# Optimization experiments

Measured on AMD Instinct MI355X. Metric: run time of the kernel, lower is better.

## Reference

```python
import jax, jax.numpy as jnp
import numpy as np

N, K, D = 65536, 1024, 256


def setup_inputs() -> dict:
    key = jax.random.key(0)
    k1, k2 = jax.random.split(key)
    e = jax.random.normal(k1, (N, D), dtype=jnp.float32)
    # module inits codebook uniform in [-1/K, 1/K]
    weight = jax.random.uniform(k2, (K, D), dtype=jnp.float32,
                                minval=-1.0 / K, maxval=1.0 / K)
    return {"e": e, "weight": weight}


def reference(e, weight):
    distances = (jnp.sum(e * e, axis=1, keepdims=True)
                 - 2.0 * jnp.matmul(e, weight.T)
                 + jnp.sum(weight * weight, axis=1))
    encoding_indices = jnp.argmin(distances, axis=1)            # [N]
    # one-hot @ weight is just a gather
    quantized = weight[encoding_indices]                        # [N, D]
    commitment_loss = jnp.mean((jax.lax.stop_gradient(quantized) - e) ** 2)
    counts = jnp.zeros((K,), dtype=jnp.float32).at[encoding_indices].add(1.0)
    codebook_usage = counts.max() / counts.sum()
    # straight-through estimator
    quantized = e + jax.lax.stop_gradient(quantized - e)
    return quantized, encoding_indices, commitment_loss, codebook_usage
```

## Files before the change

kernel.cpp:

```cpp
#include <hip/hip_runtime.h>

typedef __attribute__((ext_vector_type(8))) short short8;
typedef __attribute__((ext_vector_type(4))) float floatx4;

#define N_ROWS 65536
#define K_CB   1024
#define D_DIM  256

#define TAU 4.0e-4f
#define BLINE 520

#define OFF_WN     262144
#define OFF_FIXCNT 266240
#define OFF_HIST   266496
#define OFF_IDX    270592
#define OFF_LIST   532736
#define OFF_PART   794880
#define OFF_WFRAG  827392
#define OFF_KEYS   1351680
#define OFF_WT     1875968

__device__ __forceinline__ float pw128_sq(const float4* p) {
#pragma clang fp contract(off)
    float4 q0 = p[0], q1 = p[1];
    float r0 = q0.x * q0.x, r1 = q0.y * q0.y, r2 = q0.z * q0.z, r3 = q0.w * q0.w;
    float r4 = q1.x * q1.x, r5 = q1.y * q1.y, r6 = q1.z * q1.z, r7 = q1.w * q1.w;
    for (int i = 1; i < 16; ++i) {
        float4 u0 = p[2 * i], u1 = p[2 * i + 1];
        r0 = r0 + u0.x * u0.x; r1 = r1 + u0.y * u0.y;
        r2 = r2 + u0.z * u0.z; r3 = r3 + u0.w * u0.w;
        r4 = r4 + u1.x * u1.x; r5 = r5 + u1.y * u1.y;
        r6 = r6 + u1.z * u1.z; r7 = r7 + u1.w * u1.w;
    }
    return ((r0 + r1) + (r2 + r3)) + ((r4 + r5) + (r6 + r7));
}
__device__ __forceinline__ float rownorm_np(const float* row) {
#pragma clang fp contract(off)
    float s0 = pw128_sq((const float4*)row);
    float s1 = pw128_sq((const float4*)(row + 128));
    return s0 + s1;
}
__device__ __forceinline__ float np_dist(float A, float m, float Ck) {
#pragma clang fp contract(off)
    float Bv = 2.0f * m;
    float t  = A - Bv;
    return t + Ck;
}
__device__ __forceinline__ unsigned short bf16_rne(float x) {
    unsigned u = __float_as_uint(x);
    unsigned r = u + 0x7fff + ((u >> 16) & 1);
    return (unsigned short)(r >> 16);
}
__device__ __forceinline__ unsigned long long dist_key(float d, int idx) {
    unsigned u = __float_as_uint(d);
    unsigned k32 = u ^ (((unsigned)((int)u >> 31)) | 0x80000000u);
    return ((unsigned long long)k32 << 32) | (unsigned)idx;
}

#define PRS 260
__global__ __launch_bounds__(256) void k_prep(
        const float* __restrict__ wg,
        float* __restrict__ wn,
        unsigned short* __restrict__ wfrag, float* __restrict__ wt) {
    __shared__ __align__(16) float es[32 * PRS];
    const int tid = threadIdx.x;
    const int bx  = blockIdx.x;
    if (bx < 4) {
        int row = bx * 256 + tid;
        wn[row] = rownorm_np(wg + (size_t)row * D_DIM);
    } else if (bx < 132) {
        int t = (bx - 4) * 256 + tid;
        int col = t >> 5, kc = t & 31;
        const float4* src = (const float4*)(wg + (size_t)col * D_DIM + kc * 8);
        float4 v0 = src[0], v1 = src[1];
        const float a[8] = {v0.x, v0.y, v0.z, v0.w, v1.x, v1.y, v1.z, v1.w};
        short8 h;
        #pragma unroll
        for (int i = 0; i < 8; ++i) h[i] = (short)bf16_rne(a[i]);
        *(short8*)(wfrag + ((size_t)kc * 1024 + col) * 8) = h;
    } else {
        float (*tw)[PRS] = (float(*)[PRS])es;
        const int cb = bx - 132;
        const int c0 = cb * 32;
        #pragma unroll
        for (int it = 0; it < 8; ++it) {
            int idx = it * 256 + tid;
            int code = idx >> 6, f4 = idx & 63;
            *(float4*)&tw[code][f4 * 4] =
                *(const float4*)(wg + (size_t)(c0 + code) * D_DIM + f4 * 4);
        }
        __syncthreads();
        const int j = tid & 31, dg = tid >> 5;
        #pragma unroll
        for (int dd = 0; dd < 32; ++dd) {
            int d = dd * 8 + dg;
            wt[(size_t)d * K_CB + c0 + j] = tw[j][d];
        }
    }
}

__global__ __launch_bounds__(256, 2) void k_dist(
        const float* __restrict__ eg, const unsigned short* __restrict__ wfrag,
        const float* __restrict__ wn,
        int* __restrict__ idx_ws, int* __restrict__ fixlist, int* __restrict__ fixcnt) {
    __shared__ __align__(16) unsigned short Bs[2][32 * BLINE];
    __shared__ float wnS[K_CB];
    const int tid  = threadIdx.x;
    const int lane = tid & 63;
    const int wv   = tid >> 6;
    const int q    = lane >> 4;
    const int m15  = lane & 15;
    const int waveRow = blockIdx.x * 128 + wv * 32;

    #pragma unroll
    for (int i = 0; i < 4; ++i) wnS[tid + i * 256] = wn[tid + i * 256];

    short8 afh0[8], afh1[8];
    #pragma unroll
    for (int mt = 0; mt < 2; ++mt) {
        const float* rowp = eg + (size_t)(waveRow + mt * 16 + m15) * D_DIM + q * 8;
        #pragma unroll
        for (int win = 0; win < 8; ++win) {
            const float4* pa = (const float4*)(rowp + win * 32);
            float4 x0 = pa[0], x1 = pa[1];
            const float a[8] = {x0.x, x0.y, x0.z, x0.w, x1.x, x1.y, x1.z, x1.w};
            short8 h;
            #pragma unroll
            for (int i = 0; i < 8; ++i) h[i] = (short)bf16_rne(a[i]);
            if (mt == 0) afh0[win] = h; else afh1[win] = h;
        }
    }

    float best[8], sec[8];
    int bidx[8];
    #pragma unroll
    for (int s = 0; s < 8; ++s) { best[s] = 3.4e38f; sec[s] = 3.4e38f; bidx[s] = 0; }

    #pragma unroll
    for (int t = 0; t < 8; ++t) {
        int L = wv * 8 + t;
        const unsigned short* src = wfrag + ((size_t)L * 1024) * 8 + lane * 8;
        __builtin_amdgcn_global_load_lds(
            (const __attribute__((address_space(1))) unsigned int*)src,
            (__attribute__((address_space(3))) unsigned int*)&Bs[0][L * BLINE],
            16, 0, 0);
    }
    __syncthreads();

    for (int cb = 0; cb < 16; ++cb) {
        const int p = cb & 1;
        if (cb < 15) {
            #pragma unroll
            for (int t = 0; t < 8; ++t) {
                int L = wv * 8 + t;
                const unsigned short* src =
                    wfrag + ((size_t)L * 1024 + (cb + 1) * 64) * 8 + lane * 8;
                __builtin_amdgcn_global_load_lds(
                    (const __attribute__((address_space(1))) unsigned int*)src,
                    (__attribute__((address_space(3))) unsigned int*)&Bs[p ^ 1][L * BLINE],
                    16, 0, 0);
            }
        }
        #pragma unroll
        for (int nt = 0; nt < 4; ++nt) {
            floatx4 acc0 = (floatx4){0.f, 0.f, 0.f, 0.f};
            floatx4 acc1 = (floatx4){0.f, 0.f, 0.f, 0.f};
            #pragma unroll
            for (int win = 0; win < 8; ++win) {
                int kc = win * 4 + q;
                short8 bfh = *(short8*)&Bs[p][kc * BLINE + (nt * 16 + m15) * 8];
                acc0 = __builtin_amdgcn_mfma_f32_16x16x32_bf16(afh0[win], bfh, acc0, 0, 0, 0);
                acc1 = __builtin_amdgcn_mfma_f32_16x16x32_bf16(afh1[win], bfh, acc1, 0, 0, 0);
            }
            int col = cb * 64 + nt * 16 + m15;
            float Ck = wnS[col];
            #pragma unroll
            for (int reg = 0; reg < 4; ++reg) {
                float d0 = __builtin_fmaf(-2.0f, acc0[reg], Ck);
                bool lt0 = d0 < best[reg];
                sec[reg]  = __builtin_amdgcn_fmed3f(d0, best[reg], sec[reg]);
                best[reg] = fminf(d0, best[reg]);
                bidx[reg] = lt0 ? col : bidx[reg];
                float d1 = __builtin_fmaf(-2.0f, acc1[reg], Ck);
                int s1 = 4 + reg;
                bool lt1 = d1 < best[s1];
                sec[s1]  = __builtin_amdgcn_fmed3f(d1, best[s1], sec[s1]);
                best[s1] = fminf(d1, best[s1]);
                bidx[s1] = lt1 ? col : bidx[s1];
            }
        }
        __syncthreads();
    }

    #pragma unroll
    for (int s = 0; s < 8; ++s) {
        float b = best[s], se = sec[s];
        int ix = bidx[s];
        #pragma unroll
        for (int m = 1; m < 16; m <<= 1) {
            float bo = __shfl_xor(b, m, 64);
            float so = __shfl_xor(se, m, 64);
            int   io = __shfl_xor(ix, m, 64);
            float ns = fminf(fminf(se, so), fmaxf(b, bo));
            if (bo < b || (bo == b && io < ix)) { b = bo; ix = io; }
            se = ns;
        }
        if (m15 == 0) {
            int row = waveRow + (s >> 2) * 16 + q * 4 + (s & 3);
            idx_ws[row] = ix;
            if (se - b < TAU) {
                int p = atomicAdd(fixcnt, 1);
                fixlist[p] = row;
            }
        }
    }
}

#define FG_ROWS 8
__global__ __launch_bounds__(256) void k_fixup(
        const float* __restrict__ eg, const float* __restrict__ wg,
        const float* __restrict__ wt, const float* __restrict__ wnorm,
        const int* __restrict__ fixlist, const int* __restrict__ fixcnt,
        unsigned long long* __restrict__ keys) {
    __shared__ __align__(16) float xs[FG_ROWS][D_DIM];
    __shared__ float AnS[FG_ROWS];
    const int tid  = threadIdx.x;
    const int lane = tid & 63;
    const int cnt = *fixcnt;
    if (cnt == 0) return;
    const int ngroups = (cnt + FG_ROWS - 1) / FG_ROWS;
    const int ntiles  = ngroups * 2;
    const int rowg = tid >> 7;
    const int cg   = tid & 127;
    for (int t = blockIdx.x; t < ntiles; t += gridDim.x) {
        const int g     = t >> 1;
        const int chunk = t & 1;
        __syncthreads();
        int rows[FG_ROWS];
        #pragma unroll
        for (int i = 0; i < FG_ROWS; ++i) {
            int j = g * FG_ROWS + i;
            rows[i] = fixlist[j < cnt ? j : cnt - 1];
        }
        #pragma unroll
        for (int i = 0; i < FG_ROWS; ++i)
            xs[i][tid] = eg[(size_t)rows[i] * D_DIM + tid];
        __syncthreads();

        if (tid < 16) {
            int row = tid >> 1, half = tid & 1;
            float sN = pw128_sq((const float4*)&xs[row][half * 128]);
            float so = __shfl_xor(sN, 1, 64);
            if (half == 0) AnS[row] = sN + so;
        }

        const int c0 = chunk * 512 + cg * 4;
        float Cw[4];
        #pragma unroll
        for (int c = 0; c < 4; ++c) Cw[c] = wnorm[c0 + c];

        float s[4][4];
        #pragma unroll
        for (int r = 0; r < 4; ++r)
            #pragma unroll
            for (int c = 0; c < 4; ++c) s[r][c] = 0.f;

        #pragma unroll 2
        for (int d = 0; d < D_DIM; d += 2) {
            float4 wa = *(const float4*)(wt + (size_t)d * K_CB + c0);
            float4 wb = *(const float4*)(wt + (size_t)(d + 1) * K_CB + c0);
            #pragma unroll
            for (int r = 0; r < 4; ++r) {
                float2 e2 = *(const float2*)&xs[rowg * 4 + r][d];
                s[r][0] += e2.x * wa.x + e2.y * wb.x;
                s[r][1] += e2.x * wa.y + e2.y * wb.y;
                s[r][2] += e2.x * wa.z + e2.y * wb.z;
                s[r][3] += e2.x * wa.w + e2.y * wb.w;
            }
        }
        __syncthreads();

        #pragma unroll
        for (int r = 0; r < 4; ++r) {
            const int R = rowg * 4 + r;
            float An = AnS[R];
            unsigned long long kb = 0xFFFFFFFFFFFFFFFFull, ks = 0xFFFFFFFFFFFFFFFFull;
            #pragma unroll
            for (int c = 0; c < 4; ++c) {
                float dq = np_dist(An, s[r][c], Cw[c]);
                unsigned long long kk = dist_key(dq, c0 + c);
                if (kk < kb) { ks = kb; kb = kk; }
                else if (kk < ks) { ks = kk; }
            }
            #pragma unroll
            for (int m = 1; m < 64; m <<= 1) {
                unsigned long long ko = __shfl_xor(kb, m, 64);
                unsigned long long so = __shfl_xor(ks, m, 64);
                if (ko < kb) { ks = (so < kb) ? so : kb; kb = ko; }
                else         { ks = (ko < ks) ? ko : ks; }
            }
            int cand = (int)((lane < 32 ? kb : ks) & 0xFFFFFFFFull);
            const float* wrow = wg + (size_t)cand * D_DIM + (lane & 31) * 8;
            const float* erow = &xs[R][(lane & 31) * 8];
            double sm = 0.0;
            #pragma unroll
            for (int jj = 0; jj < 8; ++jj)
                sm += (double)erow[jj] * (double)wrow[jj];
            #pragma unroll
            for (int m = 1; m < 32; m <<= 1) sm += __shfl_xor(sm, m, 64);
            double smo = __shfl_xor(sm, 32, 64);
            if (lane == 0) {
                int i0 = (int)(kb & 0xFFFFFFFFull);
                int i1 = (int)(ks & 0xFFFFFFFFull);
                float d0 = np_dist(An, (float)sm,  wnorm[i0]);
                float d1 = np_dist(An, (float)smo, wnorm[i1]);
                unsigned long long k0 = dist_key(d0, i0);
                unsigned long long k1 = dist_key(d1, i1);
                unsigned long long kf = k0 < k1 ? k0 : k1;
                int j = g * FG_ROWS + R;
                if (j < cnt) atomicMin(&keys[j], kf);
            }
        }
    }
}

__global__ void k_fixscatter(const int* __restrict__ fixlist, const int* __restrict__ fixcnt,
                             const unsigned long long* __restrict__ keys,
                             int* __restrict__ idx_ws) {
    const int cnt = *fixcnt;
    for (int j = blockIdx.x * blockDim.x + threadIdx.x; j < cnt;
         j += gridDim.x * blockDim.x)
        idx_ws[fixlist[j]] = (int)(keys[j] & 0xFFFFFFFFull);
}

__global__ void k_final(const float* __restrict__ eg, const float* __restrict__ wg,
                        const int* __restrict__ idx_ws, float* __restrict__ qout,
                        float* __restrict__ iout, int* __restrict__ hist,
                        double* __restrict__ partials) {
    const int tid  = threadIdx.x;
    const int sub  = tid >> 6;
    const int lane = tid & 63;
    const int rowBase = blockIdx.x * 16;
    double acc = 0.0;
    #pragma unroll
    for (int g = 0; g < 4; ++g) {
        int row = rowBase + g * 4 + sub;
        int k = idx_ws[row];
        float4 ev = ((const float4*)(eg + (size_t)row * D_DIM))[lane];
        float4 wv = ((const float4*)(wg + (size_t)k   * D_DIM))[lane];
        float dx = wv.x - ev.x, dy = wv.y - ev.y, dz = wv.z - ev.z, dw = wv.w - ev.w;
        float4 qv = {ev.x + dx, ev.y + dy, ev.z + dz, ev.w + dw};
        ((float4*)(qout + (size_t)row * D_DIM))[lane] = qv;
        acc += (double)(dx * dx) + (double)(dy * dy)
             + (double)(dz * dz) + (double)(dw * dw);
        if (lane == 0) {
            iout[row] = (float)k;
            atomicAdd(&hist[k], 1);
        }
    }
    __shared__ double red[256];
    red[tid] = acc;
    __syncthreads();
    for (int st = 128; st > 0; st >>= 1) {
        if (tid < st) red[tid] += red[tid + st];
        __syncthreads();
    }
    if (tid == 0) partials[blockIdx.x] = red[0];
}

__global__ void k_scalars(const int* __restrict__ hist, const double* __restrict__ partials,
                          float* __restrict__ sout) {
    const int tid = threadIdx.x;
    double s = 0.0;
    for (int j = tid; j < N_ROWS / 16; j += 256) s += partials[j];
    int m = 0;
    for (int j = tid; j < K_CB; j += 256) m = max(m, hist[j]);
    __shared__ double rs[256];
    __shared__ int    rm[256];
    rs[tid] = s; rm[tid] = m;
    __syncthreads();
    for (int st = 128; st > 0; st >>= 1) {
        if (tid < st) { rs[tid] += rs[tid + st]; rm[tid] = max(rm[tid], rm[tid + st]); }
        __syncthreads();
    }
    if (tid == 0) {
        sout[0] = (float)(rs[0] / (double)((size_t)N_ROWS * D_DIM));
        sout[1] = (float)rm[0] / 65536.0f;
    }
}

extern "C" void kernel_launch(void* const* d_in, const int* in_sizes, int n_in,
                              void* d_out, int out_size, void* d_ws, size_t ws_size,
                              hipStream_t stream) {
    const float* e = (const float*)d_in[0];
    const float* w = (const float*)d_in[1];
    float* out  = (float*)d_out;
    float* qout = out;
    float* iout = out + (size_t)N_ROWS * D_DIM;
    float* sout = iout + N_ROWS;

    char* ws = (char*)d_ws;
    float*  wn       = (float*) (ws + OFF_WN);
    int*    fixcnt   = (int*)   (ws + OFF_FIXCNT);
    int*    hist     = (int*)   (ws + OFF_HIST);
    int*    idxp     = (int*)   (ws + OFF_IDX);
    int*    list     = (int*)   (ws + OFF_LIST);
    double* partials = (double*)(ws + OFF_PART);
    unsigned short* wfrag = (unsigned short*)(ws + OFF_WFRAG);
    unsigned long long* keys = (unsigned long long*)(ws + OFF_KEYS);
    float*  wt       = (float*) (ws + OFF_WT);

    hipMemsetAsync(ws + OFF_FIXCNT, 0, 4352, stream);
    hipMemsetAsync(ws + OFF_KEYS, 0xFF, 524288, stream);

    hipLaunchKernelGGL(k_prep,       dim3(164),         dim3(256), 0, stream, w, wn, wfrag, wt);
    hipLaunchKernelGGL(k_dist,       dim3(512),         dim3(256), 0, stream, e, wfrag, wn, idxp, list, fixcnt);
    hipLaunchKernelGGL(k_fixup,      dim3(2048),        dim3(256), 0, stream, e, w, wt, wn, list, fixcnt, keys);
    hipLaunchKernelGGL(k_fixscatter, dim3(64),          dim3(256), 0, stream, list, fixcnt, keys, idxp);
    hipLaunchKernelGGL(k_final,      dim3(N_ROWS / 16), dim3(256), 0, stream, e, w, idxp, qout, iout, hist, partials);
    hipLaunchKernelGGL(k_scalars,    dim3(1),           dim3(256), 0, stream, hist, partials, sout);
}
```

Measured before the change: 296.9 us.

## Stage e rows through LDS and interleave MFMA accumulators across column tiles

The A-fragment load now stages each wave's 16 rows into LDS with coalesced global_load_lds, replacing the strided per-lane global reads, then reads the fragments back from LDS. The MFMA loop is restructured so each B fragment feeds 8 independent accumulators (2 row tiles x 4 column tiles). This hides MFMA dependency latency and spreads the LDS reads. The cost is more accumulator registers, which may hurt occupancy under launch_bounds(256,2), plus extra barriers in the prologue.

```diff
diff --git a/kernel.cpp b/kernel.cpp
--- a/kernel.cpp
+++ b/kernel.cpp
@@ -9,6 +9,7 @@
 
 #define TAU 4.0e-4f
 #define BLINE 520
+#define PRS 260
 
 #define OFF_WN     262144
 #define OFF_FIXCNT 266240
@@ -57,7 +58,6 @@
     return ((unsigned long long)k32 << 32) | (unsigned)idx;
 }
 
-#define PRS 260
 __global__ __launch_bounds__(256) void k_prep(
         const float* __restrict__ wg,
         float* __restrict__ wn,
@@ -115,20 +115,32 @@
     #pragma unroll
     for (int i = 0; i < 4; ++i) wnS[tid + i * 256] = wn[tid + i * 256];
 
+    float* ef = (float*)&Bs[0][0];
     short8 afh0[8], afh1[8];
     #pragma unroll
     for (int mt = 0; mt < 2; ++mt) {
-        const float* rowp = eg + (size_t)(waveRow + mt * 16 + m15) * D_DIM + q * 8;
+        #pragma unroll
+        for (int t = 0; t < 16; ++t) {
+            int slot = wv * 16 + t;
+            const float* src = eg + (size_t)(waveRow + mt * 16 + t) * D_DIM + lane * 4;
+            __builtin_amdgcn_global_load_lds(
+                (const __attribute__((address_space(1))) unsigned int*)src,
+                (__attribute__((address_space(3))) unsigned int*)&ef[slot * PRS],
+                16, 0, 0);
+        }
+        __syncthreads();
+        const float* rowp = &ef[(wv * 16 + m15) * PRS + q * 8];
         #pragma unroll
         for (int win = 0; win < 8; ++win) {
-            const float4* pa = (const float4*)(rowp + win * 32);
-            float4 x0 = pa[0], x1 = pa[1];
+            float4 x0 = *(const float4*)(rowp + win * 32);
+            float4 x1 = *(const float4*)(rowp + win * 32 + 4);
             const float a[8] = {x0.x, x0.y, x0.z, x0.w, x1.x, x1.y, x1.z, x1.w};
             short8 h;
             #pragma unroll
             for (int i = 0; i < 8; ++i) h[i] = (short)bf16_rne(a[i]);
             if (mt == 0) afh0[win] = h; else afh1[win] = h;
         }
+        __syncthreads();
     }
 
     float best[8], sec[8];
@@ -161,27 +173,34 @@
                     16, 0, 0);
             }
         }
+        floatx4 acc[2][4];
+        #pragma unroll
+        for (int mt = 0; mt < 2; ++mt)
+            #pragma unroll
+            for (int nt = 0; nt < 4; ++nt)
+                acc[mt][nt] = (floatx4){0.f, 0.f, 0.f, 0.f};
+        #pragma unroll
+        for (int win = 0; win < 8; ++win) {
+            int kc = win * 4 + q;
+            #pragma unroll
+            for (int nt = 0; nt < 4; ++nt) {
+                short8 bfh = *(short8*)&Bs[p][kc * BLINE + (nt * 16 + m15) * 8];
+                acc[0][nt] = __builtin_amdgcn_mfma_f32_16x16x32_bf16(afh0[win], bfh, acc[0][nt], 0, 0, 0);
+                acc[1][nt] = __builtin_amdgcn_mfma_f32_16x16x32_bf16(afh1[win], bfh, acc[1][nt], 0, 0, 0);
+            }
+        }
         #pragma unroll
         for (int nt = 0; nt < 4; ++nt) {
-            floatx4 acc0 = (floatx4){0.f, 0.f, 0.f, 0.f};
-            floatx4 acc1 = (floatx4){0.f, 0.f, 0.f, 0.f};
-            #pragma unroll
-            for (int win = 0; win < 8; ++win) {
-                int kc = win * 4 + q;
-                short8 bfh = *(short8*)&Bs[p][kc * BLINE + (nt * 16 + m15) * 8];
-                acc0 = __builtin_amdgcn_mfma_f32_16x16x32_bf16(afh0[win], bfh, acc0, 0, 0, 0);
-                acc1 = __builtin_amdgcn_mfma_f32_16x16x32_bf16(afh1[win], bfh, acc1, 0, 0, 0);
-            }
             int col = cb * 64 + nt * 16 + m15;
             float Ck = wnS[col];
             #pragma unroll
             for (int reg = 0; reg < 4; ++reg) {
-                float d0 = __builtin_fmaf(-2.0f, acc0[reg], Ck);
+                float d0 = __builtin_fmaf(-2.0f, acc[0][nt][reg], Ck);
                 bool lt0 = d0 < best[reg];
                 sec[reg]  = __builtin_amdgcn_fmed3f(d0, best[reg], sec[reg]);
                 best[reg] = fminf(d0, best[reg]);
                 bidx[reg] = lt0 ? col : bidx[reg];
-                float d1 = __builtin_fmaf(-2.0f, acc1[reg], Ck);
+                float d1 = __builtin_fmaf(-2.0f, acc[1][nt][reg], Ck);
                 int s1 = 4 + reg;
                 bool lt1 = d1 < best[s1];
                 sec[s1]  = __builtin_amdgcn_fmed3f(d1, best[s1], sec[s1]);
```

Measured after the change: 295.9 us. Within noise of the previous version (-0.3%).
